# Optimization experiments

Hardware: AMD Instinct MI355X
Metric: run time of the kernel (lower is better)

## Reference

```python
import jax, jax.numpy as jnp
import numpy as np

B, N, D, H = 16, 1024, 384, 6
DH = D // H  # 64 per-head dim


def _layernorm(x, w, b, eps=1e-5):
    mu = jnp.mean(x, axis=-1, keepdims=True)
    var = jnp.var(x, axis=-1, keepdims=True)
    return (x - mu) * jax.lax.rsqrt(var + eps) * w + b


def setup_inputs() -> dict:
    key = jax.random.key(0)
    ks = jax.random.split(key, 10)
    std = 0.02
    return {
        "X": jax.random.normal(ks[0], (B, N, D), dtype=jnp.float32),
        "Wq": jax.random.normal(ks[1], (H, DH, D), dtype=jnp.float32) * std,
        "Wk": jax.random.normal(ks[2], (H, DH, D), dtype=jnp.float32) * std,
        "Wv": jax.random.normal(ks[3], (H, DH, D), dtype=jnp.float32) * std,
        "Wo": jax.random.normal(ks[4], (D, D), dtype=jnp.float32) * std,
        "bo": jnp.zeros((D,), dtype=jnp.float32),
        "ln1_w": jnp.ones((D,), dtype=jnp.float32),
        "ln1_b": jnp.zeros((D,), dtype=jnp.float32),
        "ln2_w": jnp.ones((D,), dtype=jnp.float32),
        "ln2_b": jnp.zeros((D,), dtype=jnp.float32),
        "W1": jax.random.normal(ks[5], (2 * D, D), dtype=jnp.float32) * std,
        "b1": jnp.zeros((2 * D,), dtype=jnp.float32),
        "W2": jax.random.normal(ks[6], (D, 2 * D), dtype=jnp.float32) * std,
        "b2": jnp.zeros((D,), dtype=jnp.float32),
    }


def reference(X, Wq, Wk, Wv, Wo, bo, ln1_w, ln1_b, ln2_w, ln2_b, W1, b1, W2, b2):
    scale = 1.0 / jnp.sqrt(jnp.float32(DH))
    # pre-LN then multi-head attention (heads vectorized, math identical to per-head loop)
    t = _layernorm(X, ln1_w, ln1_b)                       # [B,N,D]
    q = jnp.einsum('bnd,hkd->bhnk', t, Wq)                # [B,H,N,DH]
    k = jnp.einsum('bnd,hkd->bhnk', t, Wk)
    v = jnp.einsum('bnd,hkd->bhnk', t, Wv)
    scores = jnp.einsum('bhnk,bhmk->bhnm', q, k) * scale  # [B,H,N,N]
    p = jax.nn.softmax(scores, axis=-1)
    o = jnp.einsum('bhnm,bhmk->bhnk', p, v)               # [B,H,N,DH]
    o = jnp.transpose(o, (0, 2, 1, 3)).reshape(B, N, D)   # concat heads
    attn = o @ Wo.T + bo
    # residual + post-LN (dropout/drop_path are identity in eval)
    X2 = _layernorm(X + attn, ln2_w, ln2_b)
    # MLP: Linear -> exact GELU -> Linear
    h = jax.nn.gelu(X2 @ W1.T + b1, approximate=False)
    mlp = h @ W2.T + b2
    return X2 + mlp
```

## Files before the change

### kernel.cpp

```cpp
#include <hip/hip_runtime.h>
#include <math.h>

typedef float  f32x4  __attribute__((ext_vector_type(4)));
typedef __bf16 bf16x8 __attribute__((ext_vector_type(8)));
typedef __bf16 bf16x4 __attribute__((ext_vector_type(4)));

__device__ __forceinline__ void gload16(const void* g, void* l) {
  __builtin_amdgcn_global_load_lds((__attribute__((address_space(1))) const void*)g,
                                   (__attribute__((address_space(3))) void*)l, 16, 0, 0);
}

__device__ __forceinline__ f32x4 mfma16(bf16x8 a, bf16x8 b, f32x4 c) {
  return __builtin_amdgcn_mfma_f32_16x16x32_bf16(a, b, c, 0, 0, 0);
}

__device__ __forceinline__ float fast_gelu(float x) {
  const float xs = x * 0.70710678118654752f;
  const float ax = fabsf(xs);
  const float t  = __builtin_amdgcn_rcpf(1.f + 0.3275911f * ax);
  const float poly = ((((1.061405429f*t - 1.453152027f)*t + 1.421413741f)*t
                       - 0.284496736f)*t + 0.254829592f)*t;
  const float e = __builtin_amdgcn_exp2f(-1.4426950408889634f * ax * ax);
  float erfv = 1.f - poly * e;
  erfv = (xs < 0.f) ? -erfv : erfv;
  return 0.5f * x * (1.f + erfv);
}

__global__ __launch_bounds__(256) void cvt_weights(
    const float* __restrict__ Wq, const float* __restrict__ Wk, const float* __restrict__ Wv,
    const float* __restrict__ Wo, const float* __restrict__ W1, const float* __restrict__ W2,
    __bf16* __restrict__ wqkv, __bf16* __restrict__ wo, __bf16* __restrict__ w1, __bf16* __restrict__ w2)
{
  const int idx = (blockIdx.x * 256 + threadIdx.x) * 4;
  const float* src; __bf16* dst; int off;
  if      (idx < 147456) { src = Wq; dst = wqkv;          off = idx; }
  else if (idx < 294912) { src = Wk; dst = wqkv + 147456; off = idx - 147456; }
  else if (idx < 442368) { src = Wv; dst = wqkv + 294912; off = idx - 294912; }
  else if (idx < 589824) { src = Wo; dst = wo;            off = idx - 442368; }
  else if (idx < 884736) { src = W1; dst = w1;            off = idx - 589824; }
  else                   { src = W2; dst = w2;            off = idx - 884736; }
  f32x4 v = *(const f32x4*)(src + off);
  bf16x4 o = {(__bf16)v.x, (__bf16)v.y, (__bf16)v.z, (__bf16)v.w};
  *(bf16x4*)(dst + off) = o;
}

template<int MODE>
__global__ __launch_bounds__(256) void ln_kernel(
    const float* __restrict__ in, const float* __restrict__ w, const float* __restrict__ b,
    __bf16* __restrict__ outb, float* __restrict__ outf)
{
  const int row  = blockIdx.x * 4 + (threadIdx.x >> 6);
  const int lane = threadIdx.x & 63;
  const float* x = in + (size_t)row * 384;
  float v[6]; float s = 0.f;
#pragma unroll
  for (int j = 0; j < 6; ++j) { v[j] = x[lane + 64*j]; s += v[j]; }
#pragma unroll
  for (int off = 32; off > 0; off >>= 1) s += __shfl_xor(s, off);
  const float mu = s * (1.f/384.f);
  float s2 = 0.f;
#pragma unroll
  for (int j = 0; j < 6; ++j) { float d = v[j] - mu; s2 += d*d; }
#pragma unroll
  for (int off = 32; off > 0; off >>= 1) s2 += __shfl_xor(s2, off);
  const float inv = rsqrtf(s2 * (1.f/384.f) + 1e-5f);
#pragma unroll
  for (int j = 0; j < 6; ++j) {
    const int cidx = lane + 64*j;
    const float y = (v[j]-mu)*inv*w[cidx] + b[cidx];
    outb[(size_t)row*384 + cidx] = (__bf16)y;
    if constexpr (MODE == 1) outf[(size_t)row*384 + cidx] = y;
  }
}

template<int EPI, int NT, int BK>
__global__ __launch_bounds__(256, (NT == 128 && BK == 64) ? 2 : 3) void gemm_bt(
    const __bf16* __restrict__ A, const __bf16* __restrict__ Bw,
    int M, int N, int K,
    const float* __restrict__ bias, const float* __restrict__ resid,
    float* __restrict__ outf, __bf16* __restrict__ outb,
    __bf16* __restrict__ q_out, __bf16* __restrict__ k_out, __bf16* __restrict__ vt_out)
{
  constexpr int CT     = NT / 32;
  constexpr int KS     = BK / 32;
  constexpr int ASUB   = 8 * KS;
  constexpr int BSUB   = (NT / 16) * KS;
  constexpr int ROUNDS = (ASUB + BSUB) / 4;
  __shared__ __attribute__((aligned(16))) __bf16 As[2][4096 * KS];
  __shared__ __attribute__((aligned(16))) __bf16 Bs[2][NT * 32 * KS];
  const int tid  = threadIdx.x;
  const int lane = tid & 63;
  const int w    = tid >> 6;
  const int wm   = w >> 1, wn = w & 1;
  const int m0   = blockIdx.x * 128, n0 = blockIdx.y * NT;

  f32x4 acc[4][CT] = {};

  const int srow = lane & 15, skq = lane >> 4;
  const __bf16* gptr[ROUNDS];
  __bf16*       lptr[ROUNDS];
  int           lstr[ROUNDS];
#pragma unroll
  for (int r = 0; r < ROUNDS; ++r) {
    const int id = r * 4 + w;
    if (id < ASUB) {
      const int ks = id >> 3, ms = id & 7;
      gptr[r] = A + (size_t)(m0 + ms*16 + srow) * K + ks*32 + (skq << 3);
      lptr[r] = &As[0][ks * 4096 + ms * 512];
      lstr[r] = 4096 * KS;
    } else {
      const int j = id - ASUB, ks = j / (NT/16), ns = j % (NT/16);
      gptr[r] = Bw + (size_t)(n0 + ns*16 + srow) * K + ks*32 + (skq << 3);
      lptr[r] = &Bs[0][ks * (NT*32) + ns * 512];
      lstr[r] = NT * 32 * KS;
    }
  }

  auto stage = [&](int kk, int b) {
#pragma unroll
    for (int r = 0; r < ROUNDS; ++r)
      gload16(gptr[r] + kk * BK, lptr[r] + b * lstr[r]);
  };
  auto compute = [&](int b) {
#pragma unroll
    for (int ks = 0; ks < KS; ++ks) {
      bf16x8 af[4], bfr[CT];
#pragma unroll
      for (int i = 0; i < 4; ++i)
        af[i] = *(const bf16x8*)&As[b][ks*4096 + (wm*4 + i)*512 + lane*8];
#pragma unroll
      for (int j = 0; j < CT; ++j)
        bfr[j] = *(const bf16x8*)&Bs[b][ks*(NT*32) + (wn*CT + j)*512 + lane*8];
#pragma unroll
      for (int i = 0; i < 4; ++i)
#pragma unroll
        for (int j = 0; j < CT; ++j)
          acc[i][j] = mfma16(af[i], bfr[j], acc[i][j]);
    }
  };

  const int NIT = K / BK;
  stage(0, 0);
  __syncthreads();
  for (int k = 0; k < NIT; ++k) {
    const int b = k & 1;
    if (k + 1 < NIT) stage(k + 1, b ^ 1);
    compute(b);
    __syncthreads();
  }

  const int quad = lane >> 4, cc = lane & 15;
#pragma unroll
  for (int rt = 0; rt < 4; ++rt) {
#pragma unroll
    for (int ct = 0; ct < CT; ++ct) {
      const int gr0 = m0 + (wm*4 + rt)*16 + quad*4;
      const int gc  = n0 + (wn*CT + ct)*16 + cc;
      f32x4 a = acc[rt][ct];
      if constexpr (EPI == 0) {
        const int bb = gr0 >> 10, nn = gr0 & 1023;
        if (gc >= 768) {
          const int jj = gc - 768, hh = jj >> 6, dh = jj & 63;
          bf16x4 pk = {(__bf16)a[0], (__bf16)a[1], (__bf16)a[2], (__bf16)a[3]};
          *(bf16x4*)&vt_out[((size_t)((bb*6 + hh)*64 + dh) << 10) + nn] = pk;
        } else {
          const bool isq = (gc < 384);
          const int jj = isq ? gc : (gc - 384);
          __bf16* dst = isq ? q_out : k_out;
          const float sc = isq ? 0.18033688011112042f : 1.0f;
          const int hh = jj >> 6, dh = jj & 63;
#pragma unroll
          for (int i = 0; i < 4; ++i)
            dst[((size_t)(((bb*6 + hh) << 10) | (nn + i)) << 6) + dh] = (__bf16)(a[i] * sc);
        }
      } else {
#pragma unroll
        for (int i = 0; i < 4; ++i) {
          const int gr = gr0 + i;
          float val = a[i];
          if constexpr (EPI == 1) {
            const size_t idx = (size_t)gr * N + gc;
            outf[idx] = val + bias[gc] + resid[idx];
          } else if constexpr (EPI == 2) {
            outb[(size_t)gr * N + gc] = (__bf16)fast_gelu(val + bias[gc]);
          } else {
            const size_t idx = (size_t)gr * N + gc;
            outf[idx] = outf[idx] + val + bias[gc];
          }
        }
      }
    }
  }
}

__global__ __launch_bounds__(256, 3) void attn_kernel(
    const __bf16* __restrict__ qp, const __bf16* __restrict__ kp,
    const __bf16* __restrict__ vtp, __bf16* __restrict__ omat)
{
  __shared__ __attribute__((aligned(16))) __bf16 Ks[2][4096];
  __shared__ __attribute__((aligned(16))) __bf16 Vs[2][4096];
  __shared__ __attribute__((aligned(16))) __bf16 Ps[4][2][1088];
  const int tid = threadIdx.x, lane = tid & 63, w = tid >> 6;
  const int bh = blockIdx.x;
  const int q0 = blockIdx.y * 128 + w * 32;
  const int quad = lane >> 4, lo = lane & 15;

  bf16x8 qa[2][2];
#pragma unroll
  for (int t = 0; t < 2; ++t) {
    const __bf16* qb = qp + ((size_t)bh * 1024 + q0 + t*16 + lo) * 64 + (quad << 3);
    qa[t][0] = *(const bf16x8*)qb;
    qa[t][1] = *(const bf16x8*)(qb + 32);
  }

  f32x4 oacc[2][4] = {};
  float l_r[2] = {0.f, 0.f};

  auto stage = [&](int c, int bb) {
#pragma unroll
    for (int s = 0; s < 2; ++s) {
      const int ck = s * 256 + tid;
      const int l = ck & 63, g = ck >> 6;
      const int ct = g >> 1, ks = g & 1;
      const __bf16* gk = kp + ((size_t)bh*1024 + c*64 + ct*16 + (l & 15)) * 64
                            + ks*32 + ((l >> 4) << 3);
      gload16(gk, &Ks[bb][(ck & ~63) * 8]);
      const __bf16* gv = vtp + (((size_t)(bh*64 + ct*16 + (l & 15))) << 10)
                             + c*64 + ks*32 + ((l >> 4) << 3);
      gload16(gv, &Vs[bb][(ck & ~63) * 8]);
    }
  };

  stage(0, 0);
  __syncthreads();

  for (int c = 0; c < 16; ++c) {
    const int bb = c & 1;
    if (c + 1 < 16) stage(c + 1, bb ^ 1);

    f32x4 st[2][4];
#pragma unroll
    for (int ct = 0; ct < 4; ++ct) {
      bf16x8 kb0 = *(const bf16x8*)&Ks[bb][((ct*2 + 0)*64 + lane) * 8];
      bf16x8 kb1 = *(const bf16x8*)&Ks[bb][((ct*2 + 1)*64 + lane) * 8];
#pragma unroll
      for (int t = 0; t < 2; ++t) {
        f32x4 s0 = {};
        s0 = mfma16(kb0, qa[t][0], s0);
        s0 = mfma16(kb1, qa[t][1], s0);
        st[t][ct] = s0;
      }
    }
#pragma unroll
    for (int t = 0; t < 2; ++t)
#pragma unroll
      for (int ct = 0; ct < 4; ++ct) {
        const float p0 = __builtin_amdgcn_exp2f(st[t][ct][0]);
        const float p1 = __builtin_amdgcn_exp2f(st[t][ct][1]);
        const float p2 = __builtin_amdgcn_exp2f(st[t][ct][2]);
        const float p3 = __builtin_amdgcn_exp2f(st[t][ct][3]);
        l_r[t] += (p0 + p1) + (p2 + p3);
        bf16x4 pk = {(__bf16)p0, (__bf16)p1, (__bf16)p2, (__bf16)p3};
        *(bf16x4*)&Ps[w][t][lo*68 + ct*16 + quad*4] = pk;
      }
    bf16x8 pa[2][2];
#pragma unroll
    for (int t = 0; t < 2; ++t)
#pragma unroll
      for (int ks = 0; ks < 2; ++ks)
        pa[t][ks] = *(const bf16x8*)&Ps[w][t][lo*68 + ks*32 + (quad << 3)];
#pragma unroll
    for (int dt = 0; dt < 4; ++dt)
#pragma unroll
      for (int ks = 0; ks < 2; ++ks) {
        bf16x8 vb = *(const bf16x8*)&Vs[bb][((dt*2 + ks)*64 + lane) * 8];
#pragma unroll
        for (int t = 0; t < 2; ++t)
          oacc[t][dt] = mfma16(pa[t][ks], vb, oacc[t][dt]);
      }
    __syncthreads();
  }

  const int b = bh / 6, h = bh - (bh / 6) * 6;
#pragma unroll
  for (int t = 0; t < 2; ++t) {
    float ls = l_r[t];
    ls += __shfl_xor(ls, 16);
    ls += __shfl_xor(ls, 32);
#pragma unroll
    for (int i = 0; i < 4; ++i) {
      const float linv = 1.f / __shfl(ls, quad*4 + i);
      const int n = q0 + t*16 + quad*4 + i;
#pragma unroll
      for (int dt = 0; dt < 4; ++dt)
        omat[((size_t)((b << 10) | n)) * 384 + (h << 6) + dt*16 + lo] =
            (__bf16)(oacc[t][dt][i] * linv);
    }
  }
}

extern "C" void kernel_launch(void* const* d_in, const int* in_sizes, int n_in,
                              void* d_out, int out_size, void* d_ws, size_t ws_size,
                              hipStream_t stream)
{
  const float* X    = (const float*)d_in[0];
  const float* Wq   = (const float*)d_in[1];
  const float* Wk   = (const float*)d_in[2];
  const float* Wv   = (const float*)d_in[3];
  const float* Wo   = (const float*)d_in[4];
  const float* bo   = (const float*)d_in[5];
  const float* ln1w = (const float*)d_in[6];
  const float* ln1b = (const float*)d_in[7];
  const float* ln2w = (const float*)d_in[8];
  const float* ln2b = (const float*)d_in[9];
  const float* W1   = (const float*)d_in[10];
  const float* b1   = (const float*)d_in[11];
  const float* W2   = (const float*)d_in[12];
  const float* b2   = (const float*)d_in[13];

  char* ws = (char*)d_ws;
  __bf16* t_bf  = (__bf16*)(ws + 0);
  __bf16* q_bf  = (__bf16*)(ws + 12582912);
  __bf16* k_bf  = (__bf16*)(ws + 25165824);
  __bf16* omat  = (__bf16*)(ws + 37748736);
  __bf16* vt_bf = (__bf16*)(ws + 50331648);
  float*  s1    = (float*) (ws + 62914560);
  __bf16* h_bf  = (__bf16*)(ws + 62914560);
  __bf16* wqkv  = (__bf16*)(ws + 88080384);
  __bf16* wo_b  = (__bf16*)(ws + 88965120);
  __bf16* w1_b  = (__bf16*)(ws + 89260032);
  __bf16* w2_b  = (__bf16*)(ws + 89849856);
  __bf16* x2_bf = t_bf;
  float*  out   = (float*)d_out;

  cvt_weights<<<1152, 256, 0, stream>>>(Wq, Wk, Wv, Wo, W1, W2, wqkv, wo_b, w1_b, w2_b);
  ln_kernel<0><<<4096, 256, 0, stream>>>(X, ln1w, ln1b, t_bf, nullptr);
  gemm_bt<0,128,32><<<dim3(128,9), 256, 0, stream>>>(t_bf, wqkv, 16384, 1152, 384,
      nullptr, nullptr, nullptr, nullptr, q_bf, k_bf, vt_bf);
  attn_kernel<<<dim3(96,8), 256, 0, stream>>>(q_bf, k_bf, vt_bf, omat);
  gemm_bt<1,64,64><<<dim3(128,6), 256, 0, stream>>>(omat, wo_b, 16384, 384, 384,
      bo, X, s1, nullptr, nullptr, nullptr, nullptr);
  ln_kernel<1><<<4096, 256, 0, stream>>>(s1, ln2w, ln2b, x2_bf, out);
  gemm_bt<2,128,64><<<dim3(128,6), 256, 0, stream>>>(x2_bf, w1_b, 16384, 768, 384,
      b1, nullptr, nullptr, h_bf, nullptr, nullptr, nullptr);
  gemm_bt<3,64,64><<<dim3(128,6), 256, 0, stream>>>(h_bf, w2_b, 16384, 384, 768,
      b2, nullptr, out, nullptr, nullptr, nullptr, nullptr);
}
```

Baseline: 274.4 us.

## Replace LDS-staged GEMMs with register-direct loads and fuse weight cast into LN1

The GEMM kernels no longer stage A and B tiles through LDS with async global-to-LDS loads. Each wave now loads its MFMA fragments straight from global memory into registers, double-buffered across k-steps, and tile shapes change to 128 columns per block. The weight conversion and the first layernorm are merged into one launch with a block-index split, which saves a kernel launch. Dropping the LDS tiles removes the barriers and the LDS traffic. In exchange, A and B rows are reloaded by more waves without shared reuse, and the fragment loads are small strided reads.

```diff
diff --git a/kernel.cpp b/kernel.cpp
--- a/kernel.cpp
+++ b/kernel.cpp
@@ -26,25 +26,49 @@
   return 0.5f * x * (1.f + erfv);
 }
 
-__global__ __launch_bounds__(256) void cvt_weights(
+__global__ __launch_bounds__(256) void prep_kernel(
+    const float* __restrict__ X, const float* __restrict__ ln1w, const float* __restrict__ ln1b,
+    __bf16* __restrict__ t_bf,
     const float* __restrict__ Wq, const float* __restrict__ Wk, const float* __restrict__ Wv,
     const float* __restrict__ Wo, const float* __restrict__ W1, const float* __restrict__ W2,
     __bf16* __restrict__ wqkv, __bf16* __restrict__ wo, __bf16* __restrict__ w1, __bf16* __restrict__ w2)
 {
-  const int idx = (blockIdx.x * 256 + threadIdx.x) * 4;
-  const float* src; __bf16* dst; int off;
-  if      (idx < 147456) { src = Wq; dst = wqkv;          off = idx; }
-  else if (idx < 294912) { src = Wk; dst = wqkv + 147456; off = idx - 147456; }
-  else if (idx < 442368) { src = Wv; dst = wqkv + 294912; off = idx - 294912; }
-  else if (idx < 589824) { src = Wo; dst = wo;            off = idx - 442368; }
-  else if (idx < 884736) { src = W1; dst = w1;            off = idx - 589824; }
-  else                   { src = W2; dst = w2;            off = idx - 884736; }
-  f32x4 v = *(const f32x4*)(src + off);
-  bf16x4 o = {(__bf16)v.x, (__bf16)v.y, (__bf16)v.z, (__bf16)v.w};
-  *(bf16x4*)(dst + off) = o;
-}
-
-template<int MODE>
+  if (blockIdx.x >= 4096) {
+    const int idx = ((blockIdx.x - 4096) * 256 + threadIdx.x) * 4;
+    const float* src; __bf16* dst; int off;
+    if      (idx < 147456) { src = Wq; dst = wqkv;          off = idx; }
+    else if (idx < 294912) { src = Wk; dst = wqkv + 147456; off = idx - 147456; }
+    else if (idx < 442368) { src = Wv; dst = wqkv + 294912; off = idx - 294912; }
+    else if (idx < 589824) { src = Wo; dst = wo;            off = idx - 442368; }
+    else if (idx < 884736) { src = W1; dst = w1;            off = idx - 589824; }
+    else                   { src = W2; dst = w2;            off = idx - 884736; }
+    f32x4 v = *(const f32x4*)(src + off);
+    bf16x4 o = {(__bf16)v.x, (__bf16)v.y, (__bf16)v.z, (__bf16)v.w};
+    *(bf16x4*)(dst + off) = o;
+    return;
+  }
+  const int row  = blockIdx.x * 4 + (threadIdx.x >> 6);
+  const int lane = threadIdx.x & 63;
+  const float* x = X + (size_t)row * 384;
+  float v[6]; float s = 0.f;
+#pragma unroll
+  for (int j = 0; j < 6; ++j) { v[j] = x[lane + 64*j]; s += v[j]; }
+#pragma unroll
+  for (int off = 32; off > 0; off >>= 1) s += __shfl_xor(s, off);
+  const float mu = s * (1.f/384.f);
+  float s2 = 0.f;
+#pragma unroll
+  for (int j = 0; j < 6; ++j) { float d = v[j] - mu; s2 += d*d; }
+#pragma unroll
+  for (int off = 32; off > 0; off >>= 1) s2 += __shfl_xor(s2, off);
+  const float inv = rsqrtf(s2 * (1.f/384.f) + 1e-5f);
+#pragma unroll
+  for (int j = 0; j < 6; ++j) {
+    const int cidx = lane + 64*j;
+    t_bf[(size_t)row*384 + cidx] = (__bf16)((v[j]-mu)*inv*ln1w[cidx] + ln1b[cidx]);
+  }
+}
+
 __global__ __launch_bounds__(256) void ln_kernel(
     const float* __restrict__ in, const float* __restrict__ w, const float* __restrict__ b,
     __bf16* __restrict__ outb, float* __restrict__ outf)
@@ -69,93 +93,61 @@
     const int cidx = lane + 64*j;
     const float y = (v[j]-mu)*inv*w[cidx] + b[cidx];
     outb[(size_t)row*384 + cidx] = (__bf16)y;
-    if constexpr (MODE == 1) outf[(size_t)row*384 + cidx] = y;
-  }
-}
-
-template<int EPI, int NT, int BK>
-__global__ __launch_bounds__(256, (NT == 128 && BK == 64) ? 2 : 3) void gemm_bt(
-    const __bf16* __restrict__ A, const __bf16* __restrict__ Bw,
-    int M, int N, int K,
+    outf[(size_t)row*384 + cidx] = y;
+  }
+}
+
+template<int EPI, int TM, int KC>
+__global__ __launch_bounds__(256, TM == 64 ? 3 : 4) void gemm_rf(
+    const __bf16* __restrict__ A, const __bf16* __restrict__ Bw, int N,
     const float* __restrict__ bias, const float* __restrict__ resid,
     float* __restrict__ outf, __bf16* __restrict__ outb,
     __bf16* __restrict__ q_out, __bf16* __restrict__ k_out, __bf16* __restrict__ vt_out)
 {
-  constexpr int CT     = NT / 32;
-  constexpr int KS     = BK / 32;
-  constexpr int ASUB   = 8 * KS;
-  constexpr int BSUB   = (NT / 16) * KS;
-  constexpr int ROUNDS = (ASUB + BSUB) / 4;
-  __shared__ __attribute__((aligned(16))) __bf16 As[2][4096 * KS];
-  __shared__ __attribute__((aligned(16))) __bf16 Bs[2][NT * 32 * KS];
+  constexpr int MT  = TM / 16;
+  constexpr int NIT = KC / 32;
   const int tid  = threadIdx.x;
   const int lane = tid & 63;
   const int w    = tid >> 6;
   const int wm   = w >> 1, wn = w & 1;
-  const int m0   = blockIdx.x * 128, n0 = blockIdx.y * NT;
-
-  f32x4 acc[4][CT] = {};
-
-  const int srow = lane & 15, skq = lane >> 4;
-  const __bf16* gptr[ROUNDS];
-  __bf16*       lptr[ROUNDS];
-  int           lstr[ROUNDS];
-#pragma unroll
-  for (int r = 0; r < ROUNDS; ++r) {
-    const int id = r * 4 + w;
-    if (id < ASUB) {
-      const int ks = id >> 3, ms = id & 7;
-      gptr[r] = A + (size_t)(m0 + ms*16 + srow) * K + ks*32 + (skq << 3);
-      lptr[r] = &As[0][ks * 4096 + ms * 512];
-      lstr[r] = 4096 * KS;
-    } else {
-      const int j = id - ASUB, ks = j / (NT/16), ns = j % (NT/16);
-      gptr[r] = Bw + (size_t)(n0 + ns*16 + srow) * K + ks*32 + (skq << 3);
-      lptr[r] = &Bs[0][ks * (NT*32) + ns * 512];
-      lstr[r] = NT * 32 * KS;
-    }
-  }
-
-  auto stage = [&](int kk, int b) {
-#pragma unroll
-    for (int r = 0; r < ROUNDS; ++r)
-      gload16(gptr[r] + kk * BK, lptr[r] + b * lstr[r]);
+  const int m0   = blockIdx.x * (2 * TM), n0 = blockIdx.y * 128;
+  const int lo   = lane & 15, quad = lane >> 4;
+
+  const __bf16* pA = A  + (size_t)(m0 + wm*TM + lo) * KC + (quad << 3);
+  const __bf16* pB = Bw + (size_t)(n0 + wn*64 + lo) * KC + (quad << 3);
+
+  f32x4 acc[MT][4] = {};
+  bf16x8 a0[MT], b0[4], a1[MT], b1[4];
+
+  auto loadf = [&](int k, bf16x8* af, bf16x8* bf) {
+#pragma unroll
+    for (int i = 0; i < MT; ++i) af[i] = *(const bf16x8*)(pA + (size_t)i*16*KC + k*32);
+#pragma unroll
+    for (int j = 0; j < 4;  ++j) bf[j] = *(const bf16x8*)(pB + (size_t)j*16*KC + k*32);
   };
-  auto compute = [&](int b) {
-#pragma unroll
-    for (int ks = 0; ks < KS; ++ks) {
-      bf16x8 af[4], bfr[CT];
-#pragma unroll
-      for (int i = 0; i < 4; ++i)
-        af[i] = *(const bf16x8*)&As[b][ks*4096 + (wm*4 + i)*512 + lane*8];
-#pragma unroll
-      for (int j = 0; j < CT; ++j)
-        bfr[j] = *(const bf16x8*)&Bs[b][ks*(NT*32) + (wn*CT + j)*512 + lane*8];
-#pragma unroll
-      for (int i = 0; i < 4; ++i)
-#pragma unroll
-        for (int j = 0; j < CT; ++j)
-          acc[i][j] = mfma16(af[i], bfr[j], acc[i][j]);
-    }
+  auto domfma = [&](bf16x8* af, bf16x8* bf) {
+#pragma unroll
+    for (int i = 0; i < MT; ++i)
+#pragma unroll
+      for (int j = 0; j < 4; ++j)
+        acc[i][j] = mfma16(af[i], bf[j], acc[i][j]);
   };
 
-  const int NIT = K / BK;
-  stage(0, 0);
-  __syncthreads();
-  for (int k = 0; k < NIT; ++k) {
-    const int b = k & 1;
-    if (k + 1 < NIT) stage(k + 1, b ^ 1);
-    compute(b);
-    __syncthreads();
-  }
-
-  const int quad = lane >> 4, cc = lane & 15;
-#pragma unroll
-  for (int rt = 0; rt < 4; ++rt) {
-#pragma unroll
-    for (int ct = 0; ct < CT; ++ct) {
-      const int gr0 = m0 + (wm*4 + rt)*16 + quad*4;
-      const int gc  = n0 + (wn*CT + ct)*16 + cc;
+  loadf(0, a0, b0);
+  for (int k = 0; k < NIT; k += 2) {
+    loadf(k + 1, a1, b1);
+    domfma(a0, b0);
+    if (k + 2 < NIT) loadf(k + 2, a0, b0);
+    domfma(a1, b1);
+  }
+
+  const int cc = lo;
+#pragma unroll
+  for (int rt = 0; rt < MT; ++rt) {
+#pragma unroll
+    for (int ct = 0; ct < 4; ++ct) {
+      const int gr0 = m0 + wm*TM + rt*16 + quad*4;
+      const int gc  = n0 + wn*64 + ct*16 + cc;
       f32x4 a = acc[rt][ct];
       if constexpr (EPI == 0) {
         const int bb = gr0 >> 10, nn = gr0 & 1023;
@@ -333,16 +325,16 @@
   __bf16* x2_bf = t_bf;
   float*  out   = (float*)d_out;
 
-  cvt_weights<<<1152, 256, 0, stream>>>(Wq, Wk, Wv, Wo, W1, W2, wqkv, wo_b, w1_b, w2_b);
-  ln_kernel<0><<<4096, 256, 0, stream>>>(X, ln1w, ln1b, t_bf, nullptr);
-  gemm_bt<0,128,32><<<dim3(128,9), 256, 0, stream>>>(t_bf, wqkv, 16384, 1152, 384,
+  prep_kernel<<<5248, 256, 0, stream>>>(X, ln1w, ln1b, t_bf,
+      Wq, Wk, Wv, Wo, W1, W2, wqkv, wo_b, w1_b, w2_b);
+  gemm_rf<0,64,384><<<dim3(128,9), 256, 0, stream>>>(t_bf, wqkv, 1152,
       nullptr, nullptr, nullptr, nullptr, q_bf, k_bf, vt_bf);
   attn_kernel<<<dim3(96,8), 256, 0, stream>>>(q_bf, k_bf, vt_bf, omat);
-  gemm_bt<1,64,64><<<dim3(128,6), 256, 0, stream>>>(omat, wo_b, 16384, 384, 384,
+  gemm_rf<1,32,384><<<dim3(256,3), 256, 0, stream>>>(omat, wo_b, 384,
       bo, X, s1, nullptr, nullptr, nullptr, nullptr);
-  ln_kernel<1><<<4096, 256, 0, stream>>>(s1, ln2w, ln2b, x2_bf, out);
-  gemm_bt<2,128,64><<<dim3(128,6), 256, 0, stream>>>(x2_bf, w1_b, 16384, 768, 384,
+  ln_kernel<<<4096, 256, 0, stream>>>(s1, ln2w, ln2b, x2_bf, out);
+  gemm_rf<2,64,384><<<dim3(128,6), 256, 0, stream>>>(x2_bf, w1_b, 768,
       b1, nullptr, nullptr, h_bf, nullptr, nullptr, nullptr);
-  gemm_bt<3,64,64><<<dim3(128,6), 256, 0, stream>>>(h_bf, w2_b, 16384, 384, 768,
+  gemm_rf<3,32,768><<<dim3(256,3), 256, 0, stream>>>(h_bf, w2_b, 384,
       b2, nullptr, out, nullptr, nullptr, nullptr, nullptr);
 }
```

Measured after the change: 338.9 us. 23.5% more time.
